# Kernel optimization log

Measured on AMD Instinct MI355X. Metric: run time of the kernel, lower is better.

## Reference

```python
import jax, jax.numpy as jnp
import numpy as np

# Model dims (DeepSeek-V2-lite style MLA)
B, T, DIM = 1, 2048, 2048
H = 16
NOPE, ROPE, VD = 128, 64, 128
QKD = NOPE + ROPE            # 192
Q_LORA, KV_LORA = 768, 512
EPS = 1e-6
SOFTSCALE = QKD * -0.5       # faithful to source: qk_head_dim * -0.5 == -96.0 (NOT **-0.5)


def rms_norm(x, w):
    # F.rms_norm: x / sqrt(mean(x^2) + eps) * w
    return x * jax.lax.rsqrt(jnp.mean(x * x, axis=-1, keepdims=True) + EPS) * w


def apply_rope(x, freqs):
    # x: [B, T, H, D] with D even; freqs: [T, D//2] rotation angles.
    # Complex-pair rotation on interleaved (even, odd) pairs, DeepSeek style.
    b, t, h, d = x.shape
    xr = x.reshape(b, t, h, d // 2, 2)
    cos = jnp.cos(freqs)[None, :, None, :]
    sin = jnp.sin(freqs)[None, :, None, :]
    x1, x2 = xr[..., 0], xr[..., 1]
    out = jnp.stack([x1 * cos - x2 * sin, x1 * sin + x2 * cos], axis=-1)
    return out.reshape(b, t, h, d)


def setup_inputs() -> dict:
    key = jax.random.key(0)
    ks = jax.random.split(key, 8)

    def w(k, out_f, in_f):
        return jax.random.normal(k, (out_f, in_f), dtype=jnp.float32) * (in_f ** -0.5)

    x = jax.random.normal(ks[0], (B, T, DIM), dtype=jnp.float32)

    # RoPE angles: positions x inv_freq, [T, ROPE//2]
    inv_freq = 1.0 / (10000.0 ** (np.arange(0, ROPE, 2, dtype=np.float32) / ROPE))
    freqs = jnp.asarray(np.outer(np.arange(T, dtype=np.float32), inv_freq))

    # additive causal mask [T, T]
    mask = jnp.where(np.tril(np.ones((T, T), dtype=bool)), 0.0, -jnp.inf).astype(jnp.float32)

    return {
        "x": x,
        "freqs": freqs,
        "mask": mask,
        "wq_a": w(ks[1], Q_LORA, DIM),
        "q_norm_w": jnp.ones((Q_LORA,), dtype=jnp.float32),
        "wq_b": w(ks[2], H * QKD, Q_LORA),
        "wkv_a": w(ks[3], KV_LORA + ROPE, DIM),
        "kv_norm_w": jnp.ones((KV_LORA,), dtype=jnp.float32),
        "wkv_b": w(ks[4], H * (NOPE + VD), KV_LORA),
        "wo": w(ks[5], DIM, H * VD),
    }


def reference(x, freqs, mask, wq_a, q_norm_w, wq_b, wkv_a, kv_norm_w, wkv_b, wo):
    b, t, _ = x.shape

    # low-rank query path: wq_b(rms_norm(wq_a(x)))
    q = rms_norm(x @ wq_a.T, q_norm_w) @ wq_b.T            # [B,T,H*QKD]
    q = q.reshape(b, t, H, QKD)
    q_nope, q_pe = q[..., :NOPE], q[..., NOPE:]
    q_pe = apply_rope(q_pe, freqs)

    # low-rank kv path
    kv_full = x @ wkv_a.T                                  # [B,T,KV_LORA+ROPE]
    c_kv, k_pe = kv_full[..., :KV_LORA], kv_full[..., KV_LORA:]
    k_pe = apply_rope(k_pe[:, :, None, :], freqs)          # [B,T,1,ROPE]
    kv = rms_norm(c_kv, kv_norm_w) @ wkv_b.T               # [B,T,H*(NOPE+VD)]
    kv = kv.reshape(b, t, H, NOPE + VD)
    k_nope, v = kv[..., :NOPE], kv[..., NOPE:]

    qh = jnp.concatenate([q_nope, q_pe], axis=-1)          # [B,T,H,QKD]
    kh = jnp.concatenate([k_nope, jnp.broadcast_to(k_pe, (b, t, H, ROPE))], axis=-1)

    # scores [B,S,H,T]; mask.unsqueeze(1) in torch -> mask[:, None, :] here
    scores = jnp.einsum("bshd,bthd->bsht", qh, kh) * SOFTSCALE
    scores = scores + mask[:, None, :]
    attn = jax.nn.softmax(scores.astype(jnp.float32), axis=-1).astype(x.dtype)

    y = jnp.einsum("bsht,bthd->bshd", attn, v)             # [B,T,H,VD]
    out = y.reshape(b, t, H * VD) @ wo.T                   # [B,T,DIM]
    return out
```

## Files before the change

kernel.cpp:

```cpp
#include <hip/hip_runtime.h>
#include <hip/hip_bf16.h>
#include <math.h>


#define T_DIM 2048
#define HEADS 16
#define D_MODEL 2048
#define NOPE_D 128
#define ROPE_D 64
#define QKD_D 192
#define VD_D 128
#define QLORA 768
#define KVLORA 512
#define KVFULL_D 576
#define SOFTSCALE -96.0f
#define EPS_RMS 1e-6f

typedef __hip_bfloat16 bf;
typedef __attribute__((ext_vector_type(8))) short bf16x8;
typedef __attribute__((ext_vector_type(4))) float f32x4;

#define GLOAD_LDS16(gptr, lptr)                                               \
    __builtin_amdgcn_global_load_lds(                                         \
        (const __attribute__((address_space(1))) unsigned int*)(gptr),        \
        (__attribute__((address_space(3))) unsigned int*)(lptr), 16, 0, 0)

__device__ __forceinline__ void split2(float v, bf* hi, bf* lo) {
    bf h = __float2bfloat16(v);
    *hi = h;
    *lo = __float2bfloat16(v - __bfloat162float(h));
}

__global__ __launch_bounds__(256) void cvt_split(
    const float* __restrict__ in, bf* __restrict__ hi, bf* __restrict__ lo, int n)
{
    const int i = (blockIdx.x * 256 + threadIdx.x) * 4;
    if (i >= n) return;
    float4 v = *(const float4*)&in[i];
    float vv[4] = {v.x, v.y, v.z, v.w};
#pragma unroll
    for (int u = 0; u < 4; u++) split2(vv[u], &hi[i + u], &lo[i + u]);
}

__global__ __launch_bounds__(256) void cvt_hi(
    const float* __restrict__ in, bf* __restrict__ hi, int n)
{
    const int i = (blockIdx.x * 256 + threadIdx.x) * 4;
    if (i >= n) return;
    float4 v = *(const float4*)&in[i];
    hi[i + 0] = __float2bfloat16(v.x);
    hi[i + 1] = __float2bfloat16(v.y);
    hi[i + 2] = __float2bfloat16(v.z);
    hi[i + 3] = __float2bfloat16(v.w);
}

__global__ __launch_bounds__(256) void rmsnorm_cvt(
    const float* __restrict__ in, int ld, int D, const float* __restrict__ w,
    bf* __restrict__ hi, bf* __restrict__ lo)
{
    const int row = blockIdx.x;
    const float* r = in + (size_t)row * ld;
    float ss = 0.0f;
    for (int i = threadIdx.x; i < D; i += 256) { float v = r[i]; ss += v * v; }
#pragma unroll
    for (int o = 32; o > 0; o >>= 1) ss += __shfl_down(ss, o, 64);
    __shared__ float red[4];
    if ((threadIdx.x & 63) == 0) red[threadIdx.x >> 6] = ss;
    __syncthreads();
    ss = red[0] + red[1] + red[2] + red[3];
    const float scale = rsqrtf(ss / (float)D + EPS_RMS);
    for (int i = threadIdx.x; i < D; i += 256) {
        const float v = r[i] * scale * w[i];
        split2(v, &hi[(size_t)row * D + i], &lo[(size_t)row * D + i]);
    }
}

__global__ __launch_bounds__(256) void rope_k_cvt(
    const float* __restrict__ kvfull, const float* __restrict__ freqs,
    bf* __restrict__ kpeh, bf* __restrict__ kpel)
{
    const int idx = blockIdx.x * 256 + threadIdx.x;
    const int i = idx & 31, t = idx >> 5;
    const float f = freqs[t * 32 + i];
    float sn, cs; sincosf(f, &sn, &cs);
    const float x1 = kvfull[(size_t)t * KVFULL_D + KVLORA + 2 * i];
    const float x2 = kvfull[(size_t)t * KVFULL_D + KVLORA + 2 * i + 1];
    split2(x1 * cs - x2 * sn, &kpeh[t * 64 + 2 * i], &kpel[t * 64 + 2 * i]);
    split2(x1 * sn + x2 * cs, &kpeh[t * 64 + 2 * i + 1], &kpel[t * 64 + 2 * i + 1]);
}

__global__ __launch_bounds__(256) void transpose_v(
    const bf* __restrict__ vh, bf* __restrict__ vT)
{
    __shared__ bf s[32][33];
    const int t0 = blockIdx.x * 32, d0 = blockIdx.y * 32, h = blockIdx.z;
    const int tid = threadIdx.x;
    const int i = tid >> 3, j0 = (tid & 7) * 4;
    const bf* src = vh + ((size_t)(t0 + i) * 16 + h) * 128 + d0 + j0;
#pragma unroll
    for (int u = 0; u < 4; u++) s[i][j0 + u] = src[u];
    __syncthreads();
    const int jj = tid >> 3, i0 = (tid & 7) * 4;
    bf* dst = vT + ((size_t)h * 128 + d0 + jj) * 2048 + t0 + i0;
#pragma unroll
    for (int u = 0; u < 4; u++) dst[u] = s[i0 + u][jj];
}

template <int MODE>
__global__ __launch_bounds__(256) void gemm_split(
    const bf* __restrict__ Ah, const bf* __restrict__ Al,
    const bf* __restrict__ Bh, const bf* __restrict__ Bl,
    const float* __restrict__ freqs,
    float* __restrict__ Cf, bf* __restrict__ Oh, bf* __restrict__ Ol,
    bf* __restrict__ O2, int M, int N, int K)
{
    __shared__ bf sAh[128 * 32], sAl[128 * 32];
    __shared__ bf sBh[128 * 32], sBl[128 * 32];

    const int tid = threadIdx.x;
    const int lane = tid & 63, wave = tid >> 6;
    const int row0 = blockIdx.y * 128, col0 = blockIdx.x * 128;
    const int wm = (wave & 1) * 64, wn = (wave >> 1) * 64;
    const int fr = lane & 15, quad = lane >> 4;

    f32x4 acc[4][4];
#pragma unroll
    for (int i = 0; i < 4; i++)
#pragma unroll
        for (int j = 0; j < 4; j++) acc[i][j] = (f32x4){0.f, 0.f, 0.f, 0.f};

    const int trow = tid >> 2;
    const int tcol = (tid & 3) * 8;
    const size_t ldsoff = (size_t)wave * 1024;

    for (int kt = 0; kt < K; kt += 32) {
        __syncthreads();
        GLOAD_LDS16(Ah + (size_t)(row0 + trow) * K + kt + tcol,      (char*)sAh + ldsoff);
        GLOAD_LDS16(Ah + (size_t)(row0 + 64 + trow) * K + kt + tcol, (char*)sAh + 4096 + ldsoff);
        GLOAD_LDS16(Al + (size_t)(row0 + trow) * K + kt + tcol,      (char*)sAl + ldsoff);
        GLOAD_LDS16(Al + (size_t)(row0 + 64 + trow) * K + kt + tcol, (char*)sAl + 4096 + ldsoff);
        GLOAD_LDS16(Bh + (size_t)(col0 + trow) * K + kt + tcol,      (char*)sBh + ldsoff);
        GLOAD_LDS16(Bh + (size_t)(col0 + 64 + trow) * K + kt + tcol, (char*)sBh + 4096 + ldsoff);
        GLOAD_LDS16(Bl + (size_t)(col0 + trow) * K + kt + tcol,      (char*)sBl + ldsoff);
        GLOAD_LDS16(Bl + (size_t)(col0 + 64 + trow) * K + kt + tcol, (char*)sBl + 4096 + ldsoff);
        __syncthreads();

        bf16x8 a_h[4], a_l[4], b_h[4], b_l[4];
#pragma unroll
        for (int mt = 0; mt < 4; mt++) {
            const int r = (wm + mt * 16 + fr) * 32 + quad * 8;
            a_h[mt] = *(const bf16x8*)&sAh[r];
            a_l[mt] = *(const bf16x8*)&sAl[r];
        }
#pragma unroll
        for (int nt = 0; nt < 4; nt++) {
            const int r = (wn + nt * 16 + fr) * 32 + quad * 8;
            b_h[nt] = *(const bf16x8*)&sBh[r];
            b_l[nt] = *(const bf16x8*)&sBl[r];
        }
#pragma unroll
        for (int mt = 0; mt < 4; mt++)
#pragma unroll
            for (int nt = 0; nt < 4; nt++) {
                acc[mt][nt] = __builtin_amdgcn_mfma_f32_16x16x32_bf16(
                    a_l[mt], b_h[nt], acc[mt][nt], 0, 0, 0);
                acc[mt][nt] = __builtin_amdgcn_mfma_f32_16x16x32_bf16(
                    a_h[mt], b_l[nt], acc[mt][nt], 0, 0, 0);
                acc[mt][nt] = __builtin_amdgcn_mfma_f32_16x16x32_bf16(
                    a_h[mt], b_h[nt], acc[mt][nt], 0, 0, 0);
            }
    }

#pragma unroll
    for (int mt = 0; mt < 4; mt++)
#pragma unroll
        for (int nt = 0; nt < 4; nt++) {
            const int colb = col0 + wn + nt * 16;
            const int col = colb + fr;
            if (MODE == 1) {
                const int d0 = colb % 192;
                const bool rope = (d0 >= 128);
                const int ii = (d0 + fr - 128) >> 1;
#pragma unroll
                for (int r = 0; r < 4; r++) {
                    const int row = row0 + wm + mt * 16 + quad * 4 + r;
                    float v = acc[mt][nt][r];
                    if (rope) {
                        const float other = __shfl_xor(v, 1);
                        float sn, cs; sincosf(freqs[row * 32 + ii], &sn, &cs);
                        v = (fr & 1) ? (other * sn + v * cs) : (v * cs - other * sn);
                    }
                    bf h8, l8; split2(v, &h8, &l8);
                    Oh[(size_t)row * N + col] = h8;
                    Ol[(size_t)row * N + col] = l8;
                }
            } else {
                const int hh = col >> 8;
                const int d = col & 255;
#pragma unroll
                for (int r = 0; r < 4; r++) {
                    const int row = row0 + wm + mt * 16 + quad * 4 + r;
                    const float v = acc[mt][nt][r];
                    if (d < 128) {
                        bf h8, l8; split2(v, &h8, &l8);
                        Oh[(size_t)row * 2048 + hh * 128 + d] = h8;
                        Ol[(size_t)row * 2048 + hh * 128 + d] = l8;
                    } else {
                        O2[(size_t)row * 2048 + hh * 128 + (d - 128)] = __float2bfloat16(v);
                    }
                }
            }
        }
}

__global__ __launch_bounds__(256) void gemm_split64(
    const bf* __restrict__ Ah, const bf* __restrict__ Al,
    const bf* __restrict__ Bh, const bf* __restrict__ Bl,
    float* __restrict__ Cf, int M, int N, int K)
{
    __shared__ bf sAh[64 * 32], sAl[64 * 32];
    __shared__ bf sBh[64 * 32], sBl[64 * 32];

    const int tid = threadIdx.x;
    const int lane = tid & 63, wave = tid >> 6;
    const int row0 = blockIdx.y * 64, col0 = blockIdx.x * 64;
    const int wm = (wave & 1) * 32, wn = (wave >> 1) * 32;
    const int fr = lane & 15, quad = lane >> 4;

    f32x4 acc[2][2];
#pragma unroll
    for (int i = 0; i < 2; i++)
#pragma unroll
        for (int j = 0; j < 2; j++) acc[i][j] = (f32x4){0.f, 0.f, 0.f, 0.f};

    const int trow = tid >> 2;
    const int tcol = (tid & 3) * 8;
    const size_t ldsoff = (size_t)wave * 1024;

    for (int kt = 0; kt < K; kt += 32) {
        __syncthreads();
        GLOAD_LDS16(Ah + (size_t)(row0 + trow) * K + kt + tcol, (char*)sAh + ldsoff);
        GLOAD_LDS16(Al + (size_t)(row0 + trow) * K + kt + tcol, (char*)sAl + ldsoff);
        GLOAD_LDS16(Bh + (size_t)(col0 + trow) * K + kt + tcol, (char*)sBh + ldsoff);
        GLOAD_LDS16(Bl + (size_t)(col0 + trow) * K + kt + tcol, (char*)sBl + ldsoff);
        __syncthreads();

        bf16x8 a_h[2], a_l[2], b_h[2], b_l[2];
#pragma unroll
        for (int mt = 0; mt < 2; mt++) {
            const int r = (wm + mt * 16 + fr) * 32 + quad * 8;
            a_h[mt] = *(const bf16x8*)&sAh[r];
            a_l[mt] = *(const bf16x8*)&sAl[r];
        }
#pragma unroll
        for (int nt = 0; nt < 2; nt++) {
            const int r = (wn + nt * 16 + fr) * 32 + quad * 8;
            b_h[nt] = *(const bf16x8*)&sBh[r];
            b_l[nt] = *(const bf16x8*)&sBl[r];
        }
#pragma unroll
        for (int mt = 0; mt < 2; mt++)
#pragma unroll
            for (int nt = 0; nt < 2; nt++) {
                acc[mt][nt] = __builtin_amdgcn_mfma_f32_16x16x32_bf16(
                    a_l[mt], b_h[nt], acc[mt][nt], 0, 0, 0);
                acc[mt][nt] = __builtin_amdgcn_mfma_f32_16x16x32_bf16(
                    a_h[mt], b_l[nt], acc[mt][nt], 0, 0, 0);
                acc[mt][nt] = __builtin_amdgcn_mfma_f32_16x16x32_bf16(
                    a_h[mt], b_h[nt], acc[mt][nt], 0, 0, 0);
            }
    }

#pragma unroll
    for (int mt = 0; mt < 2; mt++)
#pragma unroll
        for (int nt = 0; nt < 2; nt++)
#pragma unroll
            for (int r = 0; r < 4; r++)
                Cf[(size_t)(row0 + wm + mt * 16 + quad * 4 + r) * N +
                   col0 + wn + nt * 16 + fr] = acc[mt][nt][r];
}

__global__ __launch_bounds__(256) void gemm_bf16(
    const bf* __restrict__ Ah, const bf* __restrict__ Bh,
    float* __restrict__ Cf, int M, int N, int K)
{
    __shared__ bf sAh[128 * 32];
    __shared__ bf sBh[128 * 32];

    const int tid = threadIdx.x;
    const int lane = tid & 63, wave = tid >> 6;
    const int row0 = blockIdx.y * 128, col0 = blockIdx.x * 128;
    const int wm = (wave & 1) * 64, wn = (wave >> 1) * 64;
    const int fr = lane & 15, quad = lane >> 4;

    f32x4 acc[4][4];
#pragma unroll
    for (int i = 0; i < 4; i++)
#pragma unroll
        for (int j = 0; j < 4; j++) acc[i][j] = (f32x4){0.f, 0.f, 0.f, 0.f};

    const int trow = tid >> 2;
    const int tcol = (tid & 3) * 8;
    const size_t ldsoff = (size_t)wave * 1024;

    for (int kt = 0; kt < K; kt += 32) {
        __syncthreads();
        GLOAD_LDS16(Ah + (size_t)(row0 + trow) * K + kt + tcol,      (char*)sAh + ldsoff);
        GLOAD_LDS16(Ah + (size_t)(row0 + 64 + trow) * K + kt + tcol, (char*)sAh + 4096 + ldsoff);
        GLOAD_LDS16(Bh + (size_t)(col0 + trow) * K + kt + tcol,      (char*)sBh + ldsoff);
        GLOAD_LDS16(Bh + (size_t)(col0 + 64 + trow) * K + kt + tcol, (char*)sBh + 4096 + ldsoff);
        __syncthreads();

        bf16x8 a_h[4], b_h[4];
#pragma unroll
        for (int mt = 0; mt < 4; mt++)
            a_h[mt] = *(const bf16x8*)&sAh[(wm + mt * 16 + fr) * 32 + quad * 8];
#pragma unroll
        for (int nt = 0; nt < 4; nt++)
            b_h[nt] = *(const bf16x8*)&sBh[(wn + nt * 16 + fr) * 32 + quad * 8];
#pragma unroll
        for (int mt = 0; mt < 4; mt++)
#pragma unroll
            for (int nt = 0; nt < 4; nt++)
                acc[mt][nt] = __builtin_amdgcn_mfma_f32_16x16x32_bf16(
                    a_h[mt], b_h[nt], acc[mt][nt], 0, 0, 0);
    }

#pragma unroll
    for (int mt = 0; mt < 4; mt++)
#pragma unroll
        for (int nt = 0; nt < 4; nt++)
#pragma unroll
            for (int r = 0; r < 4; r++)
                Cf[(size_t)(row0 + wm + mt * 16 + quad * 4 + r) * N +
                   col0 + wn + nt * 16 + fr] = acc[mt][nt][r];
}

__global__ __launch_bounds__(256, 2) void attn_mfma(
    const bf* __restrict__ qh, const bf* __restrict__ ql,
    const bf* __restrict__ knh, const bf* __restrict__ knl,
    const bf* __restrict__ kpeh, const bf* __restrict__ kpel,
    const bf* __restrict__ vT, bf* __restrict__ yh)
{
    const int bid = blockIdx.x;
    const int h = bid & 15;
    const int qt = (bid < 256) ? (31 - (bid >> 4)) : ((bid - 256) >> 4);

    const int tid = threadIdx.x;
    const int lane = tid & 63, wave = tid >> 6;
    const int fr = lane & 15, quad = lane >> 4;
    const int wn = wave * 32;

    __shared__ __align__(16) char smem[60416];
    bf* Ps  = (bf*)(smem + 49152);
    float* redM = (float*)(smem + 58368);
    float* redS = (float*)(smem + 59392);

    float m_i[16], l_i[16], al[16];
    f32x4 O[4][2];
#pragma unroll
    for (int i = 0; i < 16; i++) { m_i[i] = -INFINITY; l_i[i] = 0.0f; }
#pragma unroll
    for (int mt = 0; mt < 4; mt++)
#pragma unroll
        for (int nt = 0; nt < 2; nt++) O[mt][nt] = (f32x4){0.f, 0.f, 0.f, 0.f};

    const int q0 = qt * 64;
    const int nkt = ((qt + 1) * 64 + 127) >> 7;
    const int trow = tid >> 2, tcol = (tid & 3) * 8;
    const size_t loff = (size_t)wave * 1024;

    for (int kt = 0; kt < nkt; kt++) {
        const int k0 = kt * 128;
        f32x4 S[4][2];
#pragma unroll
        for (int mt = 0; mt < 4; mt++)
#pragma unroll
            for (int nt = 0; nt < 2; nt++) S[mt][nt] = (f32x4){0.f, 0.f, 0.f, 0.f};

        __syncthreads();

        for (int ch = 0; ch < 6; ch++) {
            const int d0 = ch * 32;
            char* buf = smem + ((ch & 1) ? 24576 : 0);
            GLOAD_LDS16(qh + ((size_t)(q0 + trow) * 16 + h) * 192 + d0 + tcol, buf + loff);
            GLOAD_LDS16(ql + ((size_t)(q0 + trow) * 16 + h) * 192 + d0 + tcol, buf + 4096 + loff);
            if (d0 < 128) {
                GLOAD_LDS16(knh + ((size_t)(k0 + trow) * 16 + h) * 128 + d0 + tcol,      buf + 8192 + loff);
                GLOAD_LDS16(knh + ((size_t)(k0 + 64 + trow) * 16 + h) * 128 + d0 + tcol, buf + 12288 + loff);
                GLOAD_LDS16(knl + ((size_t)(k0 + trow) * 16 + h) * 128 + d0 + tcol,      buf + 16384 + loff);
                GLOAD_LDS16(knl + ((size_t)(k0 + 64 + trow) * 16 + h) * 128 + d0 + tcol, buf + 20480 + loff);
            } else {
                GLOAD_LDS16(kpeh + (size_t)(k0 + trow) * 64 + (d0 - 128) + tcol,      buf + 8192 + loff);
                GLOAD_LDS16(kpeh + (size_t)(k0 + 64 + trow) * 64 + (d0 - 128) + tcol, buf + 12288 + loff);
                GLOAD_LDS16(kpel + (size_t)(k0 + trow) * 64 + (d0 - 128) + tcol,      buf + 16384 + loff);
                GLOAD_LDS16(kpel + (size_t)(k0 + 64 + trow) * 64 + (d0 - 128) + tcol, buf + 20480 + loff);
            }
            __syncthreads();

            const bf* sQh = (const bf*)buf;
            const bf* sQl = (const bf*)(buf + 4096);
            const bf* sKh = (const bf*)(buf + 8192);
            const bf* sKl = (const bf*)(buf + 16384);
            bf16x8 a_h[4], a_l[4], b_h[2], b_l[2];
#pragma unroll
            for (int mt = 0; mt < 4; mt++) {
                const int r = (mt * 16 + fr) * 32 + quad * 8;
                a_h[mt] = *(const bf16x8*)&sQh[r];
                a_l[mt] = *(const bf16x8*)&sQl[r];
            }
#pragma unroll
            for (int nt = 0; nt < 2; nt++) {
                const int r = (wn + nt * 16 + fr) * 32 + quad * 8;
                b_h[nt] = *(const bf16x8*)&sKh[r];
                b_l[nt] = *(const bf16x8*)&sKl[r];
            }
#pragma unroll
            for (int mt = 0; mt < 4; mt++)
#pragma unroll
                for (int nt = 0; nt < 2; nt++) {
                    S[mt][nt] = __builtin_amdgcn_mfma_f32_16x16x32_bf16(
                        a_l[mt], b_h[nt], S[mt][nt], 0, 0, 0);
                    S[mt][nt] = __builtin_amdgcn_mfma_f32_16x16x32_bf16(
                        a_h[mt], b_l[nt], S[mt][nt], 0, 0, 0);
                    S[mt][nt] = __builtin_amdgcn_mfma_f32_16x16x32_bf16(
                        a_h[mt], b_h[nt], S[mt][nt], 0, 0, 0);
                }
        }

#pragma unroll
        for (int mt = 0; mt < 4; mt++)
#pragma unroll
            for (int rr = 0; rr < 4; rr++) {
                const int ri = mt * 16 + quad * 4 + rr;
                const int rowg = q0 + ri;
                float v0 = S[mt][0][rr] * SOFTSCALE;
                float v1 = S[mt][1][rr] * SOFTSCALE;
                if (k0 + wn + fr > rowg)      v0 = -INFINITY;
                if (k0 + wn + 16 + fr > rowg) v1 = -INFINITY;
                S[mt][0][rr] = v0; S[mt][1][rr] = v1;
                float pm = fmaxf(v0, v1);
#pragma unroll
                for (int o = 1; o < 16; o <<= 1) pm = fmaxf(pm, __shfl_xor(pm, o, 64));
                if (fr == 0) redM[ri * 4 + wave] = pm;
            }
        __syncthreads();
#pragma unroll
        for (int mt = 0; mt < 4; mt++)
#pragma unroll
            for (int rr = 0; rr < 4; rr++) {
                const int idx = mt * 4 + rr;
                const int ri = mt * 16 + quad * 4 + rr;
                const float4 g = *(const float4*)&redM[ri * 4];
                const float gm = fmaxf(fmaxf(g.x, g.y), fmaxf(g.z, g.w));
                const float mn = fmaxf(m_i[idx], gm);
                al[idx] = __expf(m_i[idx] - mn);
                m_i[idx] = mn;
                const float p0 = __expf(S[mt][0][rr] - mn);
                const float p1 = __expf(S[mt][1][rr] - mn);
                S[mt][0][rr] = p0; S[mt][1][rr] = p1;
                float ps = p0 + p1;
#pragma unroll
                for (int o = 1; o < 16; o <<= 1) ps += __shfl_xor(ps, o, 64);
                if (fr == 0) redS[ri * 4 + wave] = ps;
            }
#pragma unroll
        for (int mt = 0; mt < 4; mt++)
#pragma unroll
            for (int nt = 0; nt < 2; nt++)
#pragma unroll
                for (int rr = 0; rr < 4; rr++) O[mt][nt][rr] *= al[mt * 4 + rr];
        __syncthreads();
#pragma unroll
        for (int mt = 0; mt < 4; mt++)
#pragma unroll
            for (int rr = 0; rr < 4; rr++) {
                const int idx = mt * 4 + rr;
                const int ri = mt * 16 + quad * 4 + rr;
                const float4 s4 = *(const float4*)&redS[ri * 4];
                l_i[idx] = l_i[idx] * al[idx] + (s4.x + s4.y + s4.z + s4.w);
            }

        bf* sVt = (bf*)smem;
#pragma unroll
        for (int half = 0; half < 2; half++) {
            if (half) __syncthreads();
            if ((wave >> 1) == half) {
                const int kc = wn - half * 64;
#pragma unroll
                for (int mt = 0; mt < 4; mt++)
#pragma unroll
                    for (int rr = 0; rr < 4; rr++) {
                        const int ri = mt * 16 + quad * 4 + rr;
                        Ps[ri * 72 + kc + fr]      = __float2bfloat16(S[mt][0][rr]);
                        Ps[ri * 72 + kc + 16 + fr] = __float2bfloat16(S[mt][1][rr]);
                    }
            }
            const int kb = k0 + half * 64;
            GLOAD_LDS16(vT + ((size_t)(h * 128 + trow)) * 2048 + kb + tcol,           (char*)sVt + loff);
            GLOAD_LDS16(vT + ((size_t)(h * 128 + 64 + trow)) * 2048 + kb + tcol,      (char*)sVt + 4096 + loff);
            GLOAD_LDS16(vT + ((size_t)(h * 128 + trow)) * 2048 + kb + 32 + tcol,      (char*)sVt + 8192 + loff);
            GLOAD_LDS16(vT + ((size_t)(h * 128 + 64 + trow)) * 2048 + kb + 32 + tcol, (char*)sVt + 12288 + loff);
            __syncthreads();
#pragma unroll
            for (int vc = 0; vc < 2; vc++) {
                bf16x8 ap[4], bv[2];
#pragma unroll
                for (int mt = 0; mt < 4; mt++)
                    ap[mt] = *(const bf16x8*)&Ps[(mt * 16 + fr) * 72 + vc * 32 + quad * 8];
#pragma unroll
                for (int nt = 0; nt < 2; nt++)
                    bv[nt] = *(const bf16x8*)&sVt[vc * 4096 + (wn + nt * 16 + fr) * 32 + quad * 8];
#pragma unroll
                for (int mt = 0; mt < 4; mt++)
#pragma unroll
                    for (int nt = 0; nt < 2; nt++)
                        O[mt][nt] = __builtin_amdgcn_mfma_f32_16x16x32_bf16(
                            ap[mt], bv[nt], O[mt][nt], 0, 0, 0);
            }
        }
    }

#pragma unroll
    for (int mt = 0; mt < 4; mt++)
#pragma unroll
        for (int rr = 0; rr < 4; rr++) {
            const float inv = 1.0f / l_i[mt * 4 + rr];
            const int row = q0 + mt * 16 + quad * 4 + rr;
#pragma unroll
            for (int nt = 0; nt < 2; nt++)
                yh[((size_t)row * 16 + h) * 128 + wn + nt * 16 + fr] =
                    __float2bfloat16(O[mt][nt][rr] * inv);
        }
}

extern "C" void kernel_launch(void* const* d_in, const int* in_sizes, int n_in,
                              void* d_out, int out_size, void* d_ws, size_t ws_size,
                              hipStream_t stream)
{
    const float* x        = (const float*)d_in[0];
    const float* freqs    = (const float*)d_in[1];
    const float* wq_a     = (const float*)d_in[3];
    const float* q_norm_w = (const float*)d_in[4];
    const float* wq_b     = (const float*)d_in[5];
    const float* wkv_a    = (const float*)d_in[6];
    const float* kv_norm_w= (const float*)d_in[7];
    const float* wkv_b    = (const float*)d_in[8];
    const float* wo       = (const float*)d_in[9];
    float* out            = (float*)d_out;

    char* ws = (char*)d_ws;
    bf* xh = (bf*)(ws);
    bf* xl = (bf*)(ws + 8388608);
    bf* yh = (bf*)(ws);
    bf* vT = (bf*)(ws + 8388608);
    char* AR = ws + 16777216;
    bf*    wah    = (bf*)(AR);
    bf*    wal    = (bf*)(AR + 3145728);
    float* qa     = (float*)(AR + 6291456);
    bf*    qah    = (bf*)(AR);
    bf*    qal    = (bf*)(AR + 3145728);
    bf*    wbh    = (bf*)(AR + 6291456);
    bf*    wbl    = (bf*)(AR + 11010048);
    bf*    kah    = (bf*)(AR);
    bf*    kal    = (bf*)(AR + 2359296);
    float* kvfull = (float*)(AR + 4718592);
    bf*    ckvh   = (bf*)(AR + 9437184);
    bf*    ckvl   = (bf*)(AR + 11534336);
    bf*    wvh    = (bf*)(AR);
    bf*    wvl    = (bf*)(AR + 4194304);
    bf*    woh    = (bf*)(AR);
    bf* qh   = (bf*)(ws + 33554432);
    bf* ql   = (bf*)(ws + 46137344);
    bf* knh  = (bf*)(ws + 58720256);
    bf* knl  = (bf*)(ws + 67108864);
    bf* vh   = (bf*)(ws + 75497472);
    bf* kpeh = (bf*)(ws + 83886080);
    bf* kpel = (bf*)(ws + 84148224);

    dim3 blk(256);

    cvt_split<<<4096, blk, 0, stream>>>(x, xh, xl, D_MODEL * D_MODEL);
    cvt_split<<<1536, blk, 0, stream>>>(wq_a, wah, wal, QLORA * D_MODEL);
    gemm_split64<<<dim3(12, 32), blk, 0, stream>>>(
        xh, xl, wah, wal, qa, T_DIM, QLORA, D_MODEL);
    rmsnorm_cvt<<<T_DIM, blk, 0, stream>>>(qa, QLORA, QLORA, q_norm_w, qah, qal);
    cvt_split<<<2304, blk, 0, stream>>>(wq_b, wbh, wbl, 3072 * QLORA);
    gemm_split<1><<<dim3(24, 16), blk, 0, stream>>>(
        qah, qal, wbh, wbl, freqs, nullptr, qh, ql, nullptr,
        T_DIM, 3072, QLORA);
    cvt_split<<<1152, blk, 0, stream>>>(wkv_a, kah, kal, KVFULL_D * D_MODEL);
    gemm_split64<<<dim3(9, 32), blk, 0, stream>>>(
        xh, xl, kah, kal, kvfull, T_DIM, KVFULL_D, D_MODEL);
    rope_k_cvt<<<256, blk, 0, stream>>>(kvfull, freqs, kpeh, kpel);
    rmsnorm_cvt<<<T_DIM, blk, 0, stream>>>(kvfull, KVFULL_D, KVLORA, kv_norm_w, ckvh, ckvl);
    cvt_split<<<2048, blk, 0, stream>>>(wkv_b, wvh, wvl, 4096 * KVLORA);
    gemm_split<2><<<dim3(32, 16), blk, 0, stream>>>(
        ckvh, ckvl, wvh, wvl, nullptr, nullptr, knh, knl, vh,
        T_DIM, 4096, KVLORA);
    transpose_v<<<dim3(64, 4, 16), blk, 0, stream>>>(vh, vT);
    attn_mfma<<<dim3(512), blk, 0, stream>>>(
        qh, ql, knh, knl, kpeh, kpel, vT, yh);
    cvt_hi<<<4096, blk, 0, stream>>>(wo, woh, D_MODEL * D_MODEL);
    gemm_bf16<<<dim3(16, 16), blk, 0, stream>>>(
        yh, woh, out, T_DIM, D_MODEL, D_MODEL);
}
```

Baseline: 649.6 us.

## Software-pipeline attention loads with async prefetch and explicit waitcnt barriers

Restructures the attention kernel's main loop so global-to-LDS loads for the next Q/K chunk, the V tiles and the next key tile's first chunks are issued ahead of the MFMA work that consumes the current buffers. Full __syncthreads are replaced with fine-grained vmcnt/lgkmcnt waits plus raw barriers, and a separate V buffer is added. MFMA sections are wrapped in s_setprio. The aim is to hide global memory latency behind matrix compute. In exchange LDS use rises to about 75KB per block, which may limit occupancy at two blocks per CU, and the hand-counted vmcnt values must stay exactly right.

```diff
diff --git a/kernel.cpp b/kernel.cpp
--- a/kernel.cpp
+++ b/kernel.cpp
@@ -24,6 +24,10 @@
     __builtin_amdgcn_global_load_lds(                                         \
         (const __attribute__((address_space(1))) unsigned int*)(gptr),        \
         (__attribute__((address_space(3))) unsigned int*)(lptr), 16, 0, 0)
+
+#define WAITV(N) asm volatile("s_waitcnt vmcnt(" #N ")" ::: "memory")
+#define WAITL()  asm volatile("s_waitcnt lgkmcnt(0)" ::: "memory")
+#define BARRIER() __builtin_amdgcn_s_barrier()
 
 __device__ __forceinline__ void split2(float v, bf* hi, bf* lo) {
     bf h = __float2bfloat16(v);
@@ -337,6 +341,31 @@
                    col0 + wn + nt * 16 + fr] = acc[mt][nt][r];
 }
 
+#define STAGE_QK(buf_, k0_, d0_)                                              \
+  do {                                                                        \
+    GLOAD_LDS16(qh + ((size_t)(q0 + trow) * 16 + h) * 192 + (d0_) + tcol, (buf_) + loff);          \
+    GLOAD_LDS16(ql + ((size_t)(q0 + trow) * 16 + h) * 192 + (d0_) + tcol, (buf_) + 4096 + loff);   \
+    if ((d0_) < 128) {                                                        \
+      GLOAD_LDS16(knh + ((size_t)((k0_) + trow) * 16 + h) * 128 + (d0_) + tcol,      (buf_) + 8192 + loff);  \
+      GLOAD_LDS16(knh + ((size_t)((k0_) + 64 + trow) * 16 + h) * 128 + (d0_) + tcol, (buf_) + 12288 + loff); \
+      GLOAD_LDS16(knl + ((size_t)((k0_) + trow) * 16 + h) * 128 + (d0_) + tcol,      (buf_) + 16384 + loff); \
+      GLOAD_LDS16(knl + ((size_t)((k0_) + 64 + trow) * 16 + h) * 128 + (d0_) + tcol, (buf_) + 20480 + loff); \
+    } else {                                                                  \
+      GLOAD_LDS16(kpeh + (size_t)((k0_) + trow) * 64 + (d0_) - 128 + tcol,      (buf_) + 8192 + loff);  \
+      GLOAD_LDS16(kpeh + (size_t)((k0_) + 64 + trow) * 64 + (d0_) - 128 + tcol, (buf_) + 12288 + loff); \
+      GLOAD_LDS16(kpel + (size_t)((k0_) + trow) * 64 + (d0_) - 128 + tcol,      (buf_) + 16384 + loff); \
+      GLOAD_LDS16(kpel + (size_t)((k0_) + 64 + trow) * 64 + (d0_) - 128 + tcol, (buf_) + 20480 + loff); \
+    }                                                                         \
+  } while (0)
+
+#define STAGE_V(kb_)                                                          \
+  do {                                                                        \
+    GLOAD_LDS16(vT + ((size_t)(h * 128 + trow)) * 2048 + (kb_) + tcol,           sVb + loff);          \
+    GLOAD_LDS16(vT + ((size_t)(h * 128 + 64 + trow)) * 2048 + (kb_) + tcol,      sVb + 4096 + loff);   \
+    GLOAD_LDS16(vT + ((size_t)(h * 128 + trow)) * 2048 + (kb_) + 32 + tcol,      sVb + 8192 + loff);   \
+    GLOAD_LDS16(vT + ((size_t)(h * 128 + 64 + trow)) * 2048 + (kb_) + 32 + tcol, sVb + 12288 + loff);  \
+  } while (0)
+
 __global__ __launch_bounds__(256, 2) void attn_mfma(
     const bf* __restrict__ qh, const bf* __restrict__ ql,
     const bf* __restrict__ knh, const bf* __restrict__ knl,
@@ -352,10 +381,12 @@
     const int fr = lane & 15, quad = lane >> 4;
     const int wn = wave * 32;
 
-    __shared__ __align__(16) char smem[60416];
-    bf* Ps  = (bf*)(smem + 49152);
-    float* redM = (float*)(smem + 58368);
-    float* redS = (float*)(smem + 59392);
+    __shared__ __align__(16) char smem[76800];
+    bf* Ps      = (bf*)(smem + 65536);
+    float* redM = (float*)(smem + 74752);
+    float* redS = (float*)(smem + 75776);
+    char* sVb   = smem + 49152;
+    bf* sVt     = (bf*)sVb;
 
     float m_i[16], l_i[16], al[16];
     f32x4 O[4][2];
@@ -371,34 +402,23 @@
     const int trow = tid >> 2, tcol = (tid & 3) * 8;
     const size_t loff = (size_t)wave * 1024;
 
+    STAGE_QK(smem, 0, 0);
+    STAGE_QK(smem + 24576, 0, 32);
+    WAITV(8);
+    BARRIER();
+
     for (int kt = 0; kt < nkt; kt++) {
         const int k0 = kt * 128;
+        const bool more = (kt + 1 < nkt);
         f32x4 S[4][2];
 #pragma unroll
         for (int mt = 0; mt < 4; mt++)
 #pragma unroll
             for (int nt = 0; nt < 2; nt++) S[mt][nt] = (f32x4){0.f, 0.f, 0.f, 0.f};
 
-        __syncthreads();
-
+#pragma unroll
         for (int ch = 0; ch < 6; ch++) {
-            const int d0 = ch * 32;
             char* buf = smem + ((ch & 1) ? 24576 : 0);
-            GLOAD_LDS16(qh + ((size_t)(q0 + trow) * 16 + h) * 192 + d0 + tcol, buf + loff);
-            GLOAD_LDS16(ql + ((size_t)(q0 + trow) * 16 + h) * 192 + d0 + tcol, buf + 4096 + loff);
-            if (d0 < 128) {
-                GLOAD_LDS16(knh + ((size_t)(k0 + trow) * 16 + h) * 128 + d0 + tcol,      buf + 8192 + loff);
-                GLOAD_LDS16(knh + ((size_t)(k0 + 64 + trow) * 16 + h) * 128 + d0 + tcol, buf + 12288 + loff);
-                GLOAD_LDS16(knl + ((size_t)(k0 + trow) * 16 + h) * 128 + d0 + tcol,      buf + 16384 + loff);
-                GLOAD_LDS16(knl + ((size_t)(k0 + 64 + trow) * 16 + h) * 128 + d0 + tcol, buf + 20480 + loff);
-            } else {
-                GLOAD_LDS16(kpeh + (size_t)(k0 + trow) * 64 + (d0 - 128) + tcol,      buf + 8192 + loff);
-                GLOAD_LDS16(kpeh + (size_t)(k0 + 64 + trow) * 64 + (d0 - 128) + tcol, buf + 12288 + loff);
-                GLOAD_LDS16(kpel + (size_t)(k0 + trow) * 64 + (d0 - 128) + tcol,      buf + 16384 + loff);
-                GLOAD_LDS16(kpel + (size_t)(k0 + 64 + trow) * 64 + (d0 - 128) + tcol, buf + 20480 + loff);
-            }
-            __syncthreads();
-
             const bf* sQh = (const bf*)buf;
             const bf* sQl = (const bf*)(buf + 4096);
             const bf* sKh = (const bf*)(buf + 8192);
@@ -416,6 +436,16 @@
                 b_h[nt] = *(const bf16x8*)&sKh[r];
                 b_l[nt] = *(const bf16x8*)&sKl[r];
             }
+            WAITL();
+            BARRIER();
+            if (ch < 4) {
+                STAGE_QK(buf, k0, (ch + 2) * 32);
+            } else if (ch == 4) {
+                STAGE_V(k0);
+            } else if (more) {
+                STAGE_QK(smem, k0 + 128, 0);
+            }
+            __builtin_amdgcn_s_setprio(1);
 #pragma unroll
             for (int mt = 0; mt < 4; mt++)
 #pragma unroll
@@ -427,6 +457,9 @@
                     S[mt][nt] = __builtin_amdgcn_mfma_f32_16x16x32_bf16(
                         a_h[mt], b_h[nt], S[mt][nt], 0, 0, 0);
                 }
+            __builtin_amdgcn_s_setprio(0);
+            if (ch < 4)       { WAITV(8); BARRIER(); }
+            else if (ch == 4) { WAITV(4); BARRIER(); }
         }
 
 #pragma unroll
@@ -445,7 +478,9 @@
                 for (int o = 1; o < 16; o <<= 1) pm = fmaxf(pm, __shfl_xor(pm, o, 64));
                 if (fr == 0) redM[ri * 4 + wave] = pm;
             }
-        __syncthreads();
+        if (more) STAGE_QK(smem + 24576, k0 + 128, 32);
+        WAITL();
+        BARRIER();
 #pragma unroll
         for (int mt = 0; mt < 4; mt++)
 #pragma unroll
@@ -471,7 +506,8 @@
             for (int nt = 0; nt < 2; nt++)
 #pragma unroll
                 for (int rr = 0; rr < 4; rr++) O[mt][nt][rr] *= al[mt * 4 + rr];
-        __syncthreads();
+        WAITL();
+        BARRIER();
 #pragma unroll
         for (int mt = 0; mt < 4; mt++)
 #pragma unroll
@@ -482,44 +518,78 @@
                 l_i[idx] = l_i[idx] * al[idx] + (s4.x + s4.y + s4.z + s4.w);
             }
 
-        bf* sVt = (bf*)smem;
-#pragma unroll
-        for (int half = 0; half < 2; half++) {
-            if (half) __syncthreads();
-            if ((wave >> 1) == half) {
-                const int kc = wn - half * 64;
-#pragma unroll
-                for (int mt = 0; mt < 4; mt++)
-#pragma unroll
-                    for (int rr = 0; rr < 4; rr++) {
-                        const int ri = mt * 16 + quad * 4 + rr;
-                        Ps[ri * 72 + kc + fr]      = __float2bfloat16(S[mt][0][rr]);
-                        Ps[ri * 72 + kc + 16 + fr] = __float2bfloat16(S[mt][1][rr]);
-                    }
-            }
-            const int kb = k0 + half * 64;
-            GLOAD_LDS16(vT + ((size_t)(h * 128 + trow)) * 2048 + kb + tcol,           (char*)sVt + loff);
-            GLOAD_LDS16(vT + ((size_t)(h * 128 + 64 + trow)) * 2048 + kb + tcol,      (char*)sVt + 4096 + loff);
-            GLOAD_LDS16(vT + ((size_t)(h * 128 + trow)) * 2048 + kb + 32 + tcol,      (char*)sVt + 8192 + loff);
-            GLOAD_LDS16(vT + ((size_t)(h * 128 + 64 + trow)) * 2048 + kb + 32 + tcol, (char*)sVt + 12288 + loff);
-            __syncthreads();
-#pragma unroll
-            for (int vc = 0; vc < 2; vc++) {
-                bf16x8 ap[4], bv[2];
-#pragma unroll
-                for (int mt = 0; mt < 4; mt++)
-                    ap[mt] = *(const bf16x8*)&Ps[(mt * 16 + fr) * 72 + vc * 32 + quad * 8];
+        if ((wave >> 1) == 0) {
+#pragma unroll
+            for (int mt = 0; mt < 4; mt++)
+#pragma unroll
+                for (int rr = 0; rr < 4; rr++) {
+                    const int ri = mt * 16 + quad * 4 + rr;
+                    Ps[ri * 72 + wn + fr]      = __float2bfloat16(S[mt][0][rr]);
+                    Ps[ri * 72 + wn + 16 + fr] = __float2bfloat16(S[mt][1][rr]);
+                }
+        }
+        WAITL();
+        if (more) { WAITV(16); }
+        else      { WAITV(0);  }
+        BARRIER();
+
+        bf16x8 ap[2][4], bv[2][2];
+#pragma unroll
+        for (int vc = 0; vc < 2; vc++) {
+#pragma unroll
+            for (int mt = 0; mt < 4; mt++)
+                ap[vc][mt] = *(const bf16x8*)&Ps[(mt * 16 + fr) * 72 + vc * 32 + quad * 8];
+#pragma unroll
+            for (int nt = 0; nt < 2; nt++)
+                bv[vc][nt] = *(const bf16x8*)&sVt[vc * 4096 + (wn + nt * 16 + fr) * 32 + quad * 8];
+        }
+        WAITL();
+        BARRIER();
+        STAGE_V(k0 + 64);
+        if ((wave >> 1) == 1) {
+            const int kc = wn - 64;
+#pragma unroll
+            for (int mt = 0; mt < 4; mt++)
+#pragma unroll
+                for (int rr = 0; rr < 4; rr++) {
+                    const int ri = mt * 16 + quad * 4 + rr;
+                    Ps[ri * 72 + kc + fr]      = __float2bfloat16(S[mt][0][rr]);
+                    Ps[ri * 72 + kc + 16 + fr] = __float2bfloat16(S[mt][1][rr]);
+                }
+        }
+        __builtin_amdgcn_s_setprio(1);
+#pragma unroll
+        for (int vc = 0; vc < 2; vc++)
+#pragma unroll
+            for (int mt = 0; mt < 4; mt++)
 #pragma unroll
                 for (int nt = 0; nt < 2; nt++)
-                    bv[nt] = *(const bf16x8*)&sVt[vc * 4096 + (wn + nt * 16 + fr) * 32 + quad * 8];
-#pragma unroll
-                for (int mt = 0; mt < 4; mt++)
-#pragma unroll
-                    for (int nt = 0; nt < 2; nt++)
-                        O[mt][nt] = __builtin_amdgcn_mfma_f32_16x16x32_bf16(
-                            ap[mt], bv[nt], O[mt][nt], 0, 0, 0);
-            }
-        }
+                    O[mt][nt] = __builtin_amdgcn_mfma_f32_16x16x32_bf16(
+                        ap[vc][mt], bv[vc][nt], O[mt][nt], 0, 0, 0);
+        __builtin_amdgcn_s_setprio(0);
+
+        WAITL();
+        WAITV(0);
+        BARRIER();
+#pragma unroll
+        for (int vc = 0; vc < 2; vc++) {
+#pragma unroll
+            for (int mt = 0; mt < 4; mt++)
+                ap[vc][mt] = *(const bf16x8*)&Ps[(mt * 16 + fr) * 72 + vc * 32 + quad * 8];
+#pragma unroll
+            for (int nt = 0; nt < 2; nt++)
+                bv[vc][nt] = *(const bf16x8*)&sVt[vc * 4096 + (wn + nt * 16 + fr) * 32 + quad * 8];
+        }
+        __builtin_amdgcn_s_setprio(1);
+#pragma unroll
+        for (int vc = 0; vc < 2; vc++)
+#pragma unroll
+            for (int mt = 0; mt < 4; mt++)
+#pragma unroll
+                for (int nt = 0; nt < 2; nt++)
+                    O[mt][nt] = __builtin_amdgcn_mfma_f32_16x16x32_bf16(
+                        ap[vc][mt], bv[vc][nt], O[mt][nt], 0, 0, 0);
+        __builtin_amdgcn_s_setprio(0);
     }
 
 #pragma unroll
```

Result: slower. 976.7 us (+50.4%).

## Load attention Q/K/V fragments directly from global into registers, bypassing LDS

Applied to the files above, without the earlier changes.

The attention kernel no longer stages Q, K and V tiles in shared memory with global_load_lds. Each wave now reads its MFMA operand fragments straight from global memory into registers, and V fragments are prefetched before the softmax barriers. The probability tile is widened to hold all 128 keys at once, so the two-half PV loop and most __syncthreads calls collapse into two explicit barriers. The aim is to cut LDS traffic and synchronisation. The cost is that each wave redundantly reloads the Q fragments, the loads are less coalesced and less asynchronous, and register pressure rises.

```diff
diff --git a/kernel.cpp b/kernel.cpp
--- a/kernel.cpp
+++ b/kernel.cpp
@@ -24,6 +24,9 @@
     __builtin_amdgcn_global_load_lds(                                         \
         (const __attribute__((address_space(1))) unsigned int*)(gptr),        \
         (__attribute__((address_space(3))) unsigned int*)(lptr), 16, 0, 0)
+
+#define WAITL()  asm volatile("s_waitcnt lgkmcnt(0)" ::: "memory")
+#define BARRIER() __builtin_amdgcn_s_barrier()
 
 __device__ __forceinline__ void split2(float v, bf* hi, bf* lo) {
     bf h = __float2bfloat16(v);
@@ -352,10 +355,9 @@
     const int fr = lane & 15, quad = lane >> 4;
     const int wn = wave * 32;
 
-    __shared__ __align__(16) char smem[60416];
-    bf* Ps  = (bf*)(smem + 49152);
-    float* redM = (float*)(smem + 58368);
-    float* redS = (float*)(smem + 59392);
+    __shared__ __align__(16) bf Ps[64 * 136];
+    __shared__ __align__(16) float redM[64 * 4];
+    __shared__ __align__(16) float redS[64 * 4];
 
     float m_i[16], l_i[16], al[16];
     f32x4 O[4][2];
@@ -368,8 +370,15 @@
 
     const int q0 = qt * 64;
     const int nkt = ((qt + 1) * 64 + 127) >> 7;
-    const int trow = tid >> 2, tcol = (tid & 3) * 8;
-    const size_t loff = (size_t)wave * 1024;
+
+    size_t qoff[4];
+#pragma unroll
+    for (int mt = 0; mt < 4; mt++)
+        qoff[mt] = ((size_t)(q0 + mt * 16 + fr) * 16 + h) * 192 + quad * 8;
+    size_t voff[2];
+#pragma unroll
+    for (int nt = 0; nt < 2; nt++)
+        voff[nt] = ((size_t)(h * 128 + wn + nt * 16 + fr)) * 2048 + quad * 8;
 
     for (int kt = 0; kt < nkt; kt++) {
         const int k0 = kt * 128;
@@ -379,42 +388,31 @@
 #pragma unroll
             for (int nt = 0; nt < 2; nt++) S[mt][nt] = (f32x4){0.f, 0.f, 0.f, 0.f};
 
-        __syncthreads();
-
+#pragma unroll
         for (int ch = 0; ch < 6; ch++) {
             const int d0 = ch * 32;
-            char* buf = smem + ((ch & 1) ? 24576 : 0);
-            GLOAD_LDS16(qh + ((size_t)(q0 + trow) * 16 + h) * 192 + d0 + tcol, buf + loff);
-            GLOAD_LDS16(ql + ((size_t)(q0 + trow) * 16 + h) * 192 + d0 + tcol, buf + 4096 + loff);
+            bf16x8 a_h[4], a_l[4], b_h[2], b_l[2];
+#pragma unroll
+            for (int mt = 0; mt < 4; mt++) {
+                a_h[mt] = *(const bf16x8*)&qh[qoff[mt] + d0];
+                a_l[mt] = *(const bf16x8*)&ql[qoff[mt] + d0];
+            }
             if (d0 < 128) {
-                GLOAD_LDS16(knh + ((size_t)(k0 + trow) * 16 + h) * 128 + d0 + tcol,      buf + 8192 + loff);
-                GLOAD_LDS16(knh + ((size_t)(k0 + 64 + trow) * 16 + h) * 128 + d0 + tcol, buf + 12288 + loff);
-                GLOAD_LDS16(knl + ((size_t)(k0 + trow) * 16 + h) * 128 + d0 + tcol,      buf + 16384 + loff);
-                GLOAD_LDS16(knl + ((size_t)(k0 + 64 + trow) * 16 + h) * 128 + d0 + tcol, buf + 20480 + loff);
+#pragma unroll
+                for (int nt = 0; nt < 2; nt++) {
+                    const size_t koff =
+                        ((size_t)(k0 + wn + nt * 16 + fr) * 16 + h) * 128 + d0 + quad * 8;
+                    b_h[nt] = *(const bf16x8*)&knh[koff];
+                    b_l[nt] = *(const bf16x8*)&knl[koff];
+                }
             } else {
-                GLOAD_LDS16(kpeh + (size_t)(k0 + trow) * 64 + (d0 - 128) + tcol,      buf + 8192 + loff);
-                GLOAD_LDS16(kpeh + (size_t)(k0 + 64 + trow) * 64 + (d0 - 128) + tcol, buf + 12288 + loff);
-                GLOAD_LDS16(kpel + (size_t)(k0 + trow) * 64 + (d0 - 128) + tcol,      buf + 16384 + loff);
-                GLOAD_LDS16(kpel + (size_t)(k0 + 64 + trow) * 64 + (d0 - 128) + tcol, buf + 20480 + loff);
-            }
-            __syncthreads();
-
-            const bf* sQh = (const bf*)buf;
-            const bf* sQl = (const bf*)(buf + 4096);
-            const bf* sKh = (const bf*)(buf + 8192);
-            const bf* sKl = (const bf*)(buf + 16384);
-            bf16x8 a_h[4], a_l[4], b_h[2], b_l[2];
-#pragma unroll
-            for (int mt = 0; mt < 4; mt++) {
-                const int r = (mt * 16 + fr) * 32 + quad * 8;
-                a_h[mt] = *(const bf16x8*)&sQh[r];
-                a_l[mt] = *(const bf16x8*)&sQl[r];
-            }
-#pragma unroll
-            for (int nt = 0; nt < 2; nt++) {
-                const int r = (wn + nt * 16 + fr) * 32 + quad * 8;
-                b_h[nt] = *(const bf16x8*)&sKh[r];
-                b_l[nt] = *(const bf16x8*)&sKl[r];
+#pragma unroll
+                for (int nt = 0; nt < 2; nt++) {
+                    const size_t koff =
+                        (size_t)(k0 + wn + nt * 16 + fr) * 64 + (d0 - 128) + quad * 8;
+                    b_h[nt] = *(const bf16x8*)&kpeh[koff];
+                    b_l[nt] = *(const bf16x8*)&kpel[koff];
+                }
             }
 #pragma unroll
             for (int mt = 0; mt < 4; mt++)
@@ -445,7 +443,17 @@
                 for (int o = 1; o < 16; o <<= 1) pm = fmaxf(pm, __shfl_xor(pm, o, 64));
                 if (fr == 0) redM[ri * 4 + wave] = pm;
             }
-        __syncthreads();
+
+        bf16x8 bv[4][2];
+#pragma unroll
+        for (int vc = 0; vc < 4; vc++)
+#pragma unroll
+            for (int nt = 0; nt < 2; nt++)
+                bv[vc][nt] = *(const bf16x8*)&vT[voff[nt] + k0 + vc * 32];
+
+        WAITL();
+        BARRIER();
+
 #pragma unroll
         for (int mt = 0; mt < 4; mt++)
 #pragma unroll
@@ -459,7 +467,8 @@
                 m_i[idx] = mn;
                 const float p0 = __expf(S[mt][0][rr] - mn);
                 const float p1 = __expf(S[mt][1][rr] - mn);
-                S[mt][0][rr] = p0; S[mt][1][rr] = p1;
+                Ps[ri * 136 + wn + fr]      = __float2bfloat16(p0);
+                Ps[ri * 136 + wn + 16 + fr] = __float2bfloat16(p1);
                 float ps = p0 + p1;
 #pragma unroll
                 for (int o = 1; o < 16; o <<= 1) ps += __shfl_xor(ps, o, 64);
@@ -471,7 +480,10 @@
             for (int nt = 0; nt < 2; nt++)
 #pragma unroll
                 for (int rr = 0; rr < 4; rr++) O[mt][nt][rr] *= al[mt * 4 + rr];
-        __syncthreads();
+
+        WAITL();
+        BARRIER();
+
 #pragma unroll
         for (int mt = 0; mt < 4; mt++)
 #pragma unroll
@@ -482,43 +494,18 @@
                 l_i[idx] = l_i[idx] * al[idx] + (s4.x + s4.y + s4.z + s4.w);
             }
 
-        bf* sVt = (bf*)smem;
-#pragma unroll
-        for (int half = 0; half < 2; half++) {
-            if (half) __syncthreads();
-            if ((wave >> 1) == half) {
-                const int kc = wn - half * 64;
-#pragma unroll
-                for (int mt = 0; mt < 4; mt++)
-#pragma unroll
-                    for (int rr = 0; rr < 4; rr++) {
-                        const int ri = mt * 16 + quad * 4 + rr;
-                        Ps[ri * 72 + kc + fr]      = __float2bfloat16(S[mt][0][rr]);
-                        Ps[ri * 72 + kc + 16 + fr] = __float2bfloat16(S[mt][1][rr]);
-                    }
-            }
-            const int kb = k0 + half * 64;
-            GLOAD_LDS16(vT + ((size_t)(h * 128 + trow)) * 2048 + kb + tcol,           (char*)sVt + loff);
-            GLOAD_LDS16(vT + ((size_t)(h * 128 + 64 + trow)) * 2048 + kb + tcol,      (char*)sVt + 4096 + loff);
-            GLOAD_LDS16(vT + ((size_t)(h * 128 + trow)) * 2048 + kb + 32 + tcol,      (char*)sVt + 8192 + loff);
-            GLOAD_LDS16(vT + ((size_t)(h * 128 + 64 + trow)) * 2048 + kb + 32 + tcol, (char*)sVt + 12288 + loff);
-            __syncthreads();
-#pragma unroll
-            for (int vc = 0; vc < 2; vc++) {
-                bf16x8 ap[4], bv[2];
-#pragma unroll
-                for (int mt = 0; mt < 4; mt++)
-                    ap[mt] = *(const bf16x8*)&Ps[(mt * 16 + fr) * 72 + vc * 32 + quad * 8];
+#pragma unroll
+        for (int vc = 0; vc < 4; vc++) {
+            bf16x8 ap[4];
+#pragma unroll
+            for (int mt = 0; mt < 4; mt++)
+                ap[mt] = *(const bf16x8*)&Ps[(mt * 16 + fr) * 136 + vc * 32 + quad * 8];
+#pragma unroll
+            for (int mt = 0; mt < 4; mt++)
 #pragma unroll
                 for (int nt = 0; nt < 2; nt++)
-                    bv[nt] = *(const bf16x8*)&sVt[vc * 4096 + (wn + nt * 16 + fr) * 32 + quad * 8];
-#pragma unroll
-                for (int mt = 0; mt < 4; mt++)
-#pragma unroll
-                    for (int nt = 0; nt < 2; nt++)
-                        O[mt][nt] = __builtin_amdgcn_mfma_f32_16x16x32_bf16(
-                            ap[mt], bv[nt], O[mt][nt], 0, 0, 0);
-            }
+                    O[mt][nt] = __builtin_amdgcn_mfma_f32_16x16x32_bf16(
+                        ap[mt], bv[vc][nt], O[mt][nt], 0, 0, 0);
         }
     }
 
```

New measurement: 791.9 us. 21.9% more time.
